# Performance work log

Measured on AMD Instinct MI355X. Metric: run time of the kernel, lower is better.

The kernel has to match this reference:

```python
import jax, jax.numpy as jnp
import numpy as np
import math

EMBED_DIM = 1024
NUM_HEADS = 16
HEAD_DIM = EMBED_DIM // NUM_HEADS
MAX_POSITION = 1024
BATCH = 4
SEQ_LEN = 1024


def setup_inputs() -> dict:
    key = jax.random.key(0)
    ks = jax.random.split(key, 10)
    s = 1.0 / math.sqrt(EMBED_DIM)
    inp = {
        "x": jax.random.normal(ks[0], (BATCH, SEQ_LEN, EMBED_DIM), dtype=jnp.float32),
        "Wq": jax.random.normal(ks[1], (EMBED_DIM, EMBED_DIM), dtype=jnp.float32) * s,
        "bq": jnp.zeros((EMBED_DIM,), dtype=jnp.float32),
        "Wk": jax.random.normal(ks[2], (EMBED_DIM, EMBED_DIM), dtype=jnp.float32) * s,
        "bk": jnp.zeros((EMBED_DIM,), dtype=jnp.float32),
        "Wv": jax.random.normal(ks[3], (EMBED_DIM, EMBED_DIM), dtype=jnp.float32) * s,
        "bv": jnp.zeros((EMBED_DIM,), dtype=jnp.float32),
        "Wo": jax.random.normal(ks[4], (EMBED_DIM, EMBED_DIM), dtype=jnp.float32) * s,
        "bo": jnp.zeros((EMBED_DIM,), dtype=jnp.float32),
        "rel_key": jax.random.normal(ks[5], (MAX_POSITION, HEAD_DIM), dtype=jnp.float32),
    }
    return inp


def reference(x, Wq, bq, Wk, bk, Wv, bv, Wo, bo, rel_key):
    B, S, E = x.shape
    H, D = NUM_HEADS, HEAD_DIM
    # projections, split heads -> (B, H, S, D)
    Q = (x @ Wq + bq).reshape(B, S, H, D).transpose(0, 2, 1, 3)
    K = (x @ Wk + bk).reshape(B, S, H, D).transpose(0, 2, 1, 3)
    V = (x @ Wv + bv).reshape(B, S, H, D).transpose(0, 2, 1, 3)
    # content scores
    attn_content = jnp.einsum('bhqd,bhkd->bhqk', Q, K)
    # relative-position scores via skew trick
    rel = rel_key[MAX_POSITION - S:, :]              # (S, D)
    QEr = jnp.einsum('bhqd,sd->bhqs', Q, rel)        # (B, H, S, S)
    padded = jnp.pad(QEr, ((0, 0), (0, 0), (0, 0), (1, 0)))  # (B, H, S, S+1)
    Srel = padded.reshape(B, H, S + 1, S)[:, :, 1:, :]       # (B, H, S, S)
    scores = (attn_content + Srel) * (1.0 / math.sqrt(D))
    # causal mask
    mask = jnp.tril(jnp.ones((S, S), dtype=bool))
    scores = jnp.where(mask[None, None], scores, -jnp.inf)
    w = jax.nn.softmax(scores, axis=-1)
    out = jnp.einsum('bhqk,bhkd->bhqd', w, V)
    out = out.transpose(0, 2, 1, 3).reshape(B, S, E)
    return out @ Wo + bo
```

## Files before the change

kernel.cpp:

```cpp
#include <hip/hip_runtime.h>

typedef unsigned short u16;
typedef __attribute__((ext_vector_type(8))) __bf16 bf16x8;
typedef __attribute__((ext_vector_type(4))) float f32x4;
typedef __attribute__((ext_vector_type(4))) u16 u16x4;


__device__ __forceinline__ u16 f2bf(float f) {
  unsigned u = __float_as_uint(f);
  u += 0x7fff + ((u >> 16) & 1);
  return (u16)(u >> 16);
}

__device__ __forceinline__ f32x4 mfma16(bf16x8 a, bf16x8 b, f32x4 c) {
  return __builtin_amdgcn_mfma_f32_16x16x32_bf16(a, b, c, 0, 0, 0);
}

__device__ __forceinline__ void gload16(const void* g, void* l) {
  __builtin_amdgcn_global_load_lds(
      (__attribute__((address_space(1))) unsigned int*)(const_cast<void*>(g)),
      (__attribute__((address_space(3))) unsigned int*)l, 16, 0, 0);
}


__global__ void k_f32_to_bf16(const float* __restrict__ in, u16* __restrict__ out, int n4) {
  int i = blockIdx.x * blockDim.x + threadIdx.x;
  if (i < n4) {
    float4 v = reinterpret_cast<const float4*>(in)[i];
    u16x4 o;
    o.x = f2bf(v.x); o.y = f2bf(v.y); o.z = f2bf(v.z); o.w = f2bf(v.w);
    reinterpret_cast<u16x4*>(out)[i] = o;
  }
}

__global__ void k_prep_small(const float* __restrict__ rel, u16* __restrict__ relb,
                             const float* __restrict__ bq, const float* __restrict__ bk,
                             const float* __restrict__ bv, float* __restrict__ bias) {
  const int bx = blockIdx.x, t = threadIdx.x;
  if (bx < 64) {
    int i = bx * 256 + t;
    float4 v = reinterpret_cast<const float4*>(rel)[i];
    u16x4 o;
    o.x = f2bf(v.x); o.y = f2bf(v.y); o.z = f2bf(v.z); o.w = f2bf(v.w);
    reinterpret_cast<u16x4*>(relb)[i] = o;
  } else {
    int i = (bx - 64) * 256 + t;
    if (i < 3072) bias[i] = (i < 1024) ? bq[i] : (i < 2048 ? bk[i - 1024] : bv[i - 2048]);
  }
}

__global__ void k_transpose_w4(const float* __restrict__ W0, const float* __restrict__ W1,
                               const float* __restrict__ W2, const float* __restrict__ W3,
                               u16* __restrict__ outbase) {
  __shared__ float tile[32][33];
  const int z = blockIdx.z;
  const float* in = (z == 0) ? W0 : (z == 1) ? W1 : (z == 2) ? W2 : W3;
  u16* out = outbase + (size_t)z * 1024 * 1024;
  const int r0 = blockIdx.y * 32, c0 = blockIdx.x * 32;
  const int t = threadIdx.x;
  for (int i = t; i < 1024; i += 256) {
    int r = i >> 5, c = i & 31;
    tile[r][c] = in[(size_t)(r0 + r) * 1024 + c0 + c];
  }
  __syncthreads();
  for (int i = t; i < 1024; i += 256) {
    int r = i >> 5, c = i & 31;
    out[(size_t)(c0 + r) * 1024 + r0 + c] = f2bf(tile[c][r]);
  }
}


template<int MODE>
__global__ __launch_bounds__(256) void k_gemm(
    const u16* __restrict__ A, const u16* __restrict__ B,
    const float* __restrict__ bias, void* __restrict__ Cout,
    u16* __restrict__ Vaux, int M, int N, int Kd)
{
  __shared__ u16 Alds[128 * 32];
  __shared__ u16 Blds[128 * 32];
  const int t = threadIdx.x;
  const int lane = t & 63, wid = t >> 6;
  const int wr = wid >> 1, wc = wid & 1;
  const int l15 = lane & 15, lg = lane >> 4;
  const int m0 = blockIdx.y * 128, n0 = blockIdx.x * 128;
  const int trow = t >> 2;
  const int tcol = (t & 3) * 8;

  const f32x4 fzero = {0.f, 0.f, 0.f, 0.f};
  f32x4 acc[4][4];
#pragma unroll
  for (int i = 0; i < 4; i++)
#pragma unroll
    for (int j = 0; j < 4; j++) acc[i][j] = fzero;

  const size_t aoff0 = (size_t)(m0 + trow) * Kd + tcol;
  const size_t aoff1 = (size_t)(m0 + 64 + trow) * Kd + tcol;
  const size_t boff0 = (size_t)(n0 + trow) * Kd + tcol;
  const size_t boff1 = (size_t)(n0 + 64 + trow) * Kd + tcol;
  u16* la0 = Alds + wid * 512;
  u16* la1 = Alds + 2048 + wid * 512;
  u16* lb0 = Blds + wid * 512;
  u16* lb1 = Blds + 2048 + wid * 512;

  for (int k0 = 0; k0 < Kd; k0 += 32) {
    gload16(A + aoff0 + k0, la0);
    gload16(A + aoff1 + k0, la1);
    gload16(B + boff0 + k0, lb0);
    gload16(B + boff1 + k0, lb1);
    __syncthreads();
    bf16x8 av[4], bv[4];
#pragma unroll
    for (int mi = 0; mi < 4; mi++)
      av[mi] = *reinterpret_cast<const bf16x8*>(Alds + (wr * 64 + mi * 16 + l15) * 32 + lg * 8);
#pragma unroll
    for (int ni = 0; ni < 4; ni++)
      bv[ni] = *reinterpret_cast<const bf16x8*>(Blds + (wc * 64 + ni * 16 + l15) * 32 + lg * 8);
#pragma unroll
    for (int mi = 0; mi < 4; mi++)
#pragma unroll
      for (int ni = 0; ni < 4; ni++)
        acc[mi][ni] = mfma16(av[mi], bv[ni], acc[mi][ni]);
    __syncthreads();
  }

#pragma unroll
  for (int mi = 0; mi < 4; mi++) {
#pragma unroll
    for (int ni = 0; ni < 4; ni++) {
      const int col = n0 + wc * 64 + ni * 16 + l15;
      const float bcol = bias[col];
#pragma unroll
      for (int r = 0; r < 4; r++) {
        const int row = m0 + wr * 64 + mi * 16 + lg * 4 + r;
        const float v = acc[mi][ni][r] + bcol;
        if (MODE == 0) {
          ((float*)Cout)[(size_t)row * N + col] = v;
        } else {
          if (col < 2048) {
            ((u16*)Cout)[(size_t)row * N + col] = f2bf(v);
          } else {
            const int bb = row >> 10, ss = row & 1023;
            Vaux[((size_t)bb * 1024 + (col - 2048)) * 1024 + ss] = f2bf(v);
          }
        }
      }
    }
  }
}


__global__ __launch_bounds__(256, 4) void k_attn(
    const u16* __restrict__ qkv,
    const u16* __restrict__ vt,
    const u16* __restrict__ relb,
    u16* __restrict__ Oout)
{
  __shared__ u16 Klds[64 * 64];
  __shared__ u16 Vlds[64 * 64];
  __shared__ float Sbuf[4][16 * 84];

  const int t = threadIdx.x;
  const int lane = t & 63, w = t >> 6;
  const int l15 = lane & 15, lg = lane >> 4;
  const int blk = blockIdx.x;
  const int bh = blk & 63;
  const int g = blk >> 6;
  const int jq = g >> 2, rq = g & 3;
  const int qbt = (jq == 0) ? (15 - rq) : (jq == 1) ? (8 + rq) : (jq == 2) ? (7 - rq) : rq;
  const int b = bh >> 4, h = bh & 15;
  const int qb = qbt * 64;
  const int qw = qb + w * 16;

  float* Wb = Sbuf[w];
  u16* Pb = (u16*)Sbuf[w];

  const f32x4 fzero = {0.f, 0.f, 0.f, 0.f};

  const size_t qrow = (size_t)(b * 1024 + qw + l15) * 3072 + h * 64;
  bf16x8 aQ0 = *reinterpret_cast<const bf16x8*>(qkv + qrow + lg * 8);
  bf16x8 aQ1 = *reinterpret_cast<const bf16x8*>(qkv + qrow + 32 + lg * 8);

  f32x4 oacc[4];
  float l_r[4];
#pragma unroll
  for (int r = 0; r < 4; r++) { oacc[r] = fzero; l_r[r] = 0.f; }

  const int srow = t >> 3;
  const int scb = ((t & 7) * 16) ^ ((srow & 7) << 4);
  const u16* Ks0 = qkv + (size_t)(b * 1024 + srow) * 3072 + 1024 + h * 64 + (scb >> 1);
  const u16* Ks1 = Ks0 + 32 * 3072;
  const u16* Vs0 = vt + (size_t)(bh * 64 + srow) * 1024 + (scb >> 1);
  const u16* Vs1 = Vs0 + 32 * 1024;
  u16* Kd0 = Klds + t * 8;  u16* Kd1 = Klds + (t + 256) * 8;
  u16* Vd0 = Vlds + t * 8;  u16* Vd1 = Vlds + (t + 256) * 8;

  const int nk = qbt + 1;
  const float SC = 0.125f * 1.44269504f;

  for (int kt = 0; kt < nk; kt++) {
    const int k0 = kt * 64;
    gload16(Ks0 + (size_t)k0 * 3072, Kd0);
    gload16(Ks1 + (size_t)k0 * 3072, Kd1);
    gload16(Vs0 + k0, Vd0);
    gload16(Vs1 + k0, Vd1);
    __syncthreads();

    f32x4 sc4[4];
#pragma unroll
    for (int tt = 0; tt < 4; tt++) sc4[tt] = fzero;
#pragma unroll
    for (int tt = 0; tt < 4; tt++) {
      const int row = tt * 16 + l15;
      const int sw = (row & 7) << 4;
      bf16x8 b0 = *reinterpret_cast<const bf16x8*>((const char*)Klds + row * 128 + ((lg * 16) ^ sw));
      bf16x8 b1 = *reinterpret_cast<const bf16x8*>((const char*)Klds + row * 128 + ((64 + lg * 16) ^ sw));
      sc4[tt] = mfma16(aQ0, b0, sc4[tt]);
      sc4[tt] = mfma16(aQ1, b1, sc4[tt]);
    }

    const int rbase = 1008 + k0 - qw;
#pragma unroll
    for (int wj = 0; wj < 5; wj++) {
      int rr = rbase + wj * 16 + l15;
      rr = rr < 0 ? 0 : (rr > 1023 ? 1023 : rr);
      const u16* rp = relb + rr * 64;
      bf16x8 b0 = *reinterpret_cast<const bf16x8*>(rp + lg * 8);
      bf16x8 b1 = *reinterpret_cast<const bf16x8*>(rp + 32 + lg * 8);
      f32x4 z = fzero;
      z = mfma16(aQ0, b0, z);
      z = mfma16(aQ1, b1, z);
#pragma unroll
      for (int r = 0; r < 4; r++)
        Wb[(lg * 4 + r) * 84 + wj * 16 + l15] = z[r];
    }
    __builtin_amdgcn_wave_barrier();

    float pvv[4][4];
#pragma unroll
    for (int r = 0; r < 4; r++) {
      const int rowi = lg * 4 + r;
      const int q = qw + rowi;
      const float* wrow = Wb + rowi * 84 + (15 - rowi);
#pragma unroll
      for (int tt = 0; tt < 4; tt++) {
        const int kg = k0 + tt * 16 + l15;
        float s = (sc4[tt][r] + wrow[tt * 16 + l15]) * SC;
        s = (kg <= q) ? s : -1e30f;
        float p = exp2f(s);
        pvv[tt][r] = p;
        l_r[r] += p;
      }
    }
    __builtin_amdgcn_wave_barrier();
    asm volatile("" ::: "memory");

#pragma unroll
    for (int tt = 0; tt < 4; tt++)
#pragma unroll
      for (int r = 0; r < 4; r++) {
        const int rowi = lg * 4 + r;
        const int cb = (32 * tt + 2 * l15) ^ ((rowi & 7) << 4);
        *(u16*)((char*)Pb + rowi * 128 + cb) = f2bf(pvv[tt][r]);
      }
    __builtin_amdgcn_wave_barrier();

#pragma unroll
    for (int s = 0; s < 2; s++) {
      const int acb = (s * 64 + lg * 16) ^ ((l15 & 7) << 4);
      bf16x8 aP = *reinterpret_cast<const bf16x8*>((const char*)Pb + l15 * 128 + acb);
#pragma unroll
      for (int dt = 0; dt < 4; dt++) {
        const int vrow = dt * 16 + l15;
        const int vcb = (s * 64 + lg * 16) ^ ((vrow & 7) << 4);
        bf16x8 bV = *reinterpret_cast<const bf16x8*>((const char*)Vlds + vrow * 128 + vcb);
        oacc[dt] = mfma16(aP, bV, oacc[dt]);
      }
    }
    __syncthreads();
  }

#pragma unroll
  for (int r = 0; r < 4; r++) {
    float l = l_r[r];
#pragma unroll
    for (int xm = 1; xm < 16; xm <<= 1) l += __shfl_xor(l, xm);
    const float inv = 1.f / l;
    const int q = qw + lg * 4 + r;
#pragma unroll
    for (int dt = 0; dt < 4; dt++)
      Oout[(size_t)(b * 1024 + q) * 1024 + h * 64 + dt * 16 + l15] = f2bf(oacc[dt][r] * inv);
  }
}


extern "C" void kernel_launch(void* const* d_in, const int* in_sizes, int n_in,
                              void* d_out, int out_size, void* d_ws, size_t ws_size,
                              hipStream_t stream) {
  const float* x   = (const float*)d_in[0];
  const float* Wq  = (const float*)d_in[1];
  const float* bq  = (const float*)d_in[2];
  const float* Wk  = (const float*)d_in[3];
  const float* bk  = (const float*)d_in[4];
  const float* Wv  = (const float*)d_in[5];
  const float* bv  = (const float*)d_in[6];
  const float* Wo  = (const float*)d_in[7];
  const float* bo  = (const float*)d_in[8];
  const float* rel = (const float*)d_in[9];

  const size_t MB = 1024 * 1024;
  char* ws = (char*)d_ws;
  u16*   xb    = (u16*)(ws);
  u16*   Wt    = (u16*)(ws + 8 * MB);
  u16*   qkvb  = (u16*)(ws + 16 * MB);
  u16*   vtb   = (u16*)(ws + 40 * MB);
  u16*   relbb = (u16*)(ws + 48 * MB);
  float* bqkv  = (float*)(ws + 49 * MB);
  u16*   Ob    = xb;

  k_f32_to_bf16<<<4096, 256, 0, stream>>>(x, xb, 1048576);
  k_prep_small<<<76, 256, 0, stream>>>(rel, relbb, bq, bk, bv, bqkv);
  k_transpose_w4<<<dim3(32, 32, 4), 256, 0, stream>>>(Wq, Wk, Wv, Wo, Wt);

  k_gemm<2><<<dim3(24, 32), 256, 0, stream>>>(xb, Wt, bqkv, qkvb, vtb, 4096, 3072, 1024);

  k_attn<<<1024, 256, 0, stream>>>(qkvb, vtb, relbb, Ob);

  k_gemm<0><<<dim3(8, 32), 256, 0, stream>>>(Ob, Wt + 3 * MB, bo, d_out, nullptr, 4096, 1024, 1024);
}
```

Measured before the change: 150.2 us.

## Double-buffer K/V/rel tiles in LDS and replace skew buffer with shuffles

The attention kernel now prefetches the next K, V and relative-position key tiles into double-buffered LDS while the current tile is computed, instead of loading and then synchronizing each iteration. The relative-key rows are staged in LDS with a swizzle, replacing per-lane global loads. The skew of the relative scores is done with lane shuffles rather than a round trip through an LDS scratch buffer, and probabilities are written straight to LDS. LDS use roughly doubles, so launch bounds drop to 2 blocks per CU, which trades occupancy for latency hiding.

```diff
diff --git a/kernel.cpp b/kernel.cpp
--- a/kernel.cpp
+++ b/kernel.cpp
@@ -149,15 +149,16 @@
 }
 
 
-__global__ __launch_bounds__(256, 4) void k_attn(
+__global__ __launch_bounds__(256, 2) void k_attn(
     const u16* __restrict__ qkv,
     const u16* __restrict__ vt,
     const u16* __restrict__ relb,
     u16* __restrict__ Oout)
 {
-  __shared__ u16 Klds[64 * 64];
-  __shared__ u16 Vlds[64 * 64];
-  __shared__ float Sbuf[4][16 * 84];
+  __shared__ u16 Klds[2][64 * 64];
+  __shared__ u16 Vlds[2][64 * 64];
+  __shared__ u16 Rlds[2][128 * 64];
+  __shared__ u16 Plds[4][16 * 64];
 
   const int t = threadIdx.x;
   const int lane = t & 63, w = t >> 6;
@@ -171,9 +172,7 @@
   const int qb = qbt * 64;
   const int qw = qb + w * 16;
 
-  float* Wb = Sbuf[w];
-  u16* Pb = (u16*)Sbuf[w];
-
+  u16* Pb = Plds[w];
   const f32x4 fzero = {0.f, 0.f, 0.f, 0.f};
 
   const size_t qrow = (size_t)(b * 1024 + qw + l15) * 3072 + h * 64;
@@ -191,20 +190,54 @@
   const u16* Ks1 = Ks0 + 32 * 3072;
   const u16* Vs0 = vt + (size_t)(bh * 64 + srow) * 1024 + (scb >> 1);
   const u16* Vs1 = Vs0 + 32 * 1024;
-  u16* Kd0 = Klds + t * 8;  u16* Kd1 = Klds + (t + 256) * 8;
-  u16* Vd0 = Vlds + t * 8;  u16* Vd1 = Vlds + (t + 256) * 8;
+
+  const int rstart = 1008 - qb - 48;
+  int rrow[4], rcol[4];
+#pragma unroll
+  for (int ci = 0; ci < 4; ci++) {
+    const int c = t + 256 * ci;
+    rrow[ci] = rstart + (c >> 3);
+    rcol[ci] = ((((c & 7) * 16) ^ (((c >> 3) & 7) << 4)) >> 1);
+  }
 
   const int nk = qbt + 1;
   const float SC = 0.125f * 1.44269504f;
 
+  gload16(Ks0, Klds[0] + t * 8);
+  gload16(Ks1, Klds[0] + (t + 256) * 8);
+  gload16(Vs0, Vlds[0] + t * 8);
+  gload16(Vs1, Vlds[0] + (t + 256) * 8);
+#pragma unroll
+  for (int ci = 0; ci < 4; ci++) {
+    int pr = rrow[ci];
+    pr = pr < 0 ? 0 : (pr > 1023 ? 1023 : pr);
+    gload16(relb + (size_t)pr * 64 + rcol[ci], Rlds[0] + (t + 256 * ci) * 8);
+  }
+  __syncthreads();
+
+  int cur = 0;
   for (int kt = 0; kt < nk; kt++) {
     const int k0 = kt * 64;
-    gload16(Ks0 + (size_t)k0 * 3072, Kd0);
-    gload16(Ks1 + (size_t)k0 * 3072, Kd1);
-    gload16(Vs0 + k0, Vd0);
-    gload16(Vs1 + k0, Vd1);
-    __syncthreads();
-
+
+    if (kt + 1 < nk) {
+      const int kn = k0 + 64;
+      u16* kb = Klds[cur ^ 1];
+      u16* vb = Vlds[cur ^ 1];
+      u16* rb = Rlds[cur ^ 1];
+      gload16(Ks0 + (size_t)kn * 3072, kb + t * 8);
+      gload16(Ks1 + (size_t)kn * 3072, kb + (t + 256) * 8);
+      gload16(Vs0 + kn, vb + t * 8);
+      gload16(Vs1 + kn, vb + (t + 256) * 8);
+#pragma unroll
+      for (int ci = 0; ci < 4; ci++) {
+        int pr = rrow[ci] + kn;
+        pr = pr < 0 ? 0 : (pr > 1023 ? 1023 : pr);
+        gload16(relb + (size_t)pr * 64 + rcol[ci], rb + (t + 256 * ci) * 8);
+      }
+    }
+
+
+    const char* Kb = (const char*)Klds[cur];
     f32x4 sc4[4];
 #pragma unroll
     for (int tt = 0; tt < 4; tt++) sc4[tt] = fzero;
@@ -212,58 +245,50 @@
     for (int tt = 0; tt < 4; tt++) {
       const int row = tt * 16 + l15;
       const int sw = (row & 7) << 4;
-      bf16x8 b0 = *reinterpret_cast<const bf16x8*>((const char*)Klds + row * 128 + ((lg * 16) ^ sw));
-      bf16x8 b1 = *reinterpret_cast<const bf16x8*>((const char*)Klds + row * 128 + ((64 + lg * 16) ^ sw));
+      bf16x8 b0 = *reinterpret_cast<const bf16x8*>(Kb + row * 128 + ((lg * 16) ^ sw));
+      bf16x8 b1 = *reinterpret_cast<const bf16x8*>(Kb + row * 128 + ((64 + lg * 16) ^ sw));
       sc4[tt] = mfma16(aQ0, b0, sc4[tt]);
       sc4[tt] = mfma16(aQ1, b1, sc4[tt]);
     }
 
-    const int rbase = 1008 + k0 - qw;
+    const char* Rb = (const char*)Rlds[cur];
+    f32x4 z[5];
 #pragma unroll
     for (int wj = 0; wj < 5; wj++) {
-      int rr = rbase + wj * 16 + l15;
-      rr = rr < 0 ? 0 : (rr > 1023 ? 1023 : rr);
-      const u16* rp = relb + rr * 64;
-      bf16x8 b0 = *reinterpret_cast<const bf16x8*>(rp + lg * 8);
-      bf16x8 b1 = *reinterpret_cast<const bf16x8*>(rp + 32 + lg * 8);
-      f32x4 z = fzero;
-      z = mfma16(aQ0, b0, z);
-      z = mfma16(aQ1, b1, z);
-#pragma unroll
-      for (int r = 0; r < 4; r++)
-        Wb[(lg * 4 + r) * 84 + wj * 16 + l15] = z[r];
-    }
-    __builtin_amdgcn_wave_barrier();
-
-    float pvv[4][4];
+      const int pr = 48 - 16 * w + wj * 16 + l15;
+      const int sw = (pr & 7) << 4;
+      bf16x8 b0 = *reinterpret_cast<const bf16x8*>(Rb + pr * 128 + ((lg * 16) ^ sw));
+      bf16x8 b1 = *reinterpret_cast<const bf16x8*>(Rb + pr * 128 + ((64 + lg * 16) ^ sw));
+      f32x4 zz = fzero;
+      zz = mfma16(aQ0, b0, zz);
+      zz = mfma16(aQ1, b1, zz);
+      z[wj] = zz;
+    }
+
 #pragma unroll
     for (int r = 0; r < 4; r++) {
       const int rowi = lg * 4 + r;
       const int q = qw + rowi;
-      const float* wrow = Wb + rowi * 84 + (15 - rowi);
+      const int u = l15 + 15 - rowi;
+      const int src = (lane & 48) | (u & 15);
+      float sz[5];
+#pragma unroll
+      for (int wj = 0; wj < 5; wj++) sz[wj] = __shfl(z[wj][r], src);
 #pragma unroll
       for (int tt = 0; tt < 4; tt++) {
         const int kg = k0 + tt * 16 + l15;
-        float s = (sc4[tt][r] + wrow[tt * 16 + l15]) * SC;
-        s = (kg <= q) ? s : -1e30f;
-        float p = exp2f(s);
-        pvv[tt][r] = p;
+        const float wv = (u & 16) ? sz[tt + 1] : sz[tt];
+        const float s = (sc4[tt][r] + wv) * SC;
+        const float p = (kg <= q) ? exp2f(s) : 0.f;
         l_r[r] += p;
+        const int cb = (32 * tt + 2 * l15) ^ ((rowi & 7) << 4);
+        *(u16*)((char*)Pb + rowi * 128 + cb) = f2bf(p);
       }
     }
     __builtin_amdgcn_wave_barrier();
     asm volatile("" ::: "memory");
 
-#pragma unroll
-    for (int tt = 0; tt < 4; tt++)
-#pragma unroll
-      for (int r = 0; r < 4; r++) {
-        const int rowi = lg * 4 + r;
-        const int cb = (32 * tt + 2 * l15) ^ ((rowi & 7) << 4);
-        *(u16*)((char*)Pb + rowi * 128 + cb) = f2bf(pvv[tt][r]);
-      }
-    __builtin_amdgcn_wave_barrier();
-
+    const char* Vb = (const char*)Vlds[cur];
 #pragma unroll
     for (int s = 0; s < 2; s++) {
       const int acb = (s * 64 + lg * 16) ^ ((l15 & 7) << 4);
@@ -272,11 +297,12 @@
       for (int dt = 0; dt < 4; dt++) {
         const int vrow = dt * 16 + l15;
         const int vcb = (s * 64 + lg * 16) ^ ((vrow & 7) << 4);
-        bf16x8 bV = *reinterpret_cast<const bf16x8*>((const char*)Vlds + vrow * 128 + vcb);
+        bf16x8 bV = *reinterpret_cast<const bf16x8*>(Vb + vrow * 128 + vcb);
         oacc[dt] = mfma16(aP, bV, oacc[dt]);
       }
     }
     __syncthreads();
+    cur ^= 1;
   }
 
 #pragma unroll
```

New measurement: 180.1 us. +19.9%, slower.

## Halve attention block to 32 queries and compute rel-pos skew via lane shuffles

Applied to the files above, without the earlier changes.

The attention kernel now uses 128-thread blocks covering 32 query rows each and launches twice as many blocks, processed in descending order of causal work. The relative-position skew, previously done by writing fp32 scores to shared memory and reading them back, is now done with cross-lane shuffles, so the fp32 scratch buffer shrinks to a small bf16 P tile. Exp and the bf16 store to P are fused into one loop. This lowers shared-memory use and improves causal load balance, at the cost of each block reloading K/V tiles for fewer queries, which raises total global traffic.

```diff
diff --git a/kernel.cpp b/kernel.cpp
--- a/kernel.cpp
+++ b/kernel.cpp
@@ -149,7 +149,7 @@
 }
 
 
-__global__ __launch_bounds__(256, 4) void k_attn(
+__global__ __launch_bounds__(128, 4) void k_attn(
     const u16* __restrict__ qkv,
     const u16* __restrict__ vt,
     const u16* __restrict__ relb,
@@ -157,7 +157,7 @@
 {
   __shared__ u16 Klds[64 * 64];
   __shared__ u16 Vlds[64 * 64];
-  __shared__ float Sbuf[4][16 * 84];
+  __shared__ u16 Plds[2][16 * 64];
 
   const int t = threadIdx.x;
   const int lane = t & 63, w = t >> 6;
@@ -165,15 +165,12 @@
   const int blk = blockIdx.x;
   const int bh = blk & 63;
   const int g = blk >> 6;
-  const int jq = g >> 2, rq = g & 3;
-  const int qbt = (jq == 0) ? (15 - rq) : (jq == 1) ? (8 + rq) : (jq == 2) ? (7 - rq) : rq;
+  const int j = 31 - g;
   const int b = bh >> 4, h = bh & 15;
-  const int qb = qbt * 64;
+  const int qb = j * 32;
   const int qw = qb + w * 16;
 
-  float* Wb = Sbuf[w];
-  u16* Pb = (u16*)Sbuf[w];
-
+  u16* Pb = Plds[w];
   const f32x4 fzero = {0.f, 0.f, 0.f, 0.f};
 
   const size_t qrow = (size_t)(b * 1024 + qw + l15) * 3072 + h * 64;
@@ -188,21 +185,18 @@
   const int srow = t >> 3;
   const int scb = ((t & 7) * 16) ^ ((srow & 7) << 4);
   const u16* Ks0 = qkv + (size_t)(b * 1024 + srow) * 3072 + 1024 + h * 64 + (scb >> 1);
-  const u16* Ks1 = Ks0 + 32 * 3072;
   const u16* Vs0 = vt + (size_t)(bh * 64 + srow) * 1024 + (scb >> 1);
-  const u16* Vs1 = Vs0 + 32 * 1024;
-  u16* Kd0 = Klds + t * 8;  u16* Kd1 = Klds + (t + 256) * 8;
-  u16* Vd0 = Vlds + t * 8;  u16* Vd1 = Vlds + (t + 256) * 8;
-
-  const int nk = qbt + 1;
+
+  const int nk = (j >> 1) + 1;
   const float SC = 0.125f * 1.44269504f;
 
   for (int kt = 0; kt < nk; kt++) {
     const int k0 = kt * 64;
-    gload16(Ks0 + (size_t)k0 * 3072, Kd0);
-    gload16(Ks1 + (size_t)k0 * 3072, Kd1);
-    gload16(Vs0 + k0, Vd0);
-    gload16(Vs1 + k0, Vd1);
+#pragma unroll
+    for (int ci = 0; ci < 4; ci++) {
+      gload16(Ks0 + (size_t)(k0 + 16 * ci) * 3072, Klds + (t + 128 * ci) * 8);
+      gload16(Vs0 + (size_t)(16384 * ci) + k0,     Vlds + (t + 128 * ci) * 8);
+    }
     __syncthreads();
 
     f32x4 sc4[4];
@@ -219,6 +213,7 @@
     }
 
     const int rbase = 1008 + k0 - qw;
+    f32x4 z[5];
 #pragma unroll
     for (int wj = 0; wj < 5; wj++) {
       int rr = rbase + wj * 16 + l15;
@@ -226,43 +221,34 @@
       const u16* rp = relb + rr * 64;
       bf16x8 b0 = *reinterpret_cast<const bf16x8*>(rp + lg * 8);
       bf16x8 b1 = *reinterpret_cast<const bf16x8*>(rp + 32 + lg * 8);
-      f32x4 z = fzero;
-      z = mfma16(aQ0, b0, z);
-      z = mfma16(aQ1, b1, z);
-#pragma unroll
-      for (int r = 0; r < 4; r++)
-        Wb[(lg * 4 + r) * 84 + wj * 16 + l15] = z[r];
-    }
-    __builtin_amdgcn_wave_barrier();
-
-    float pvv[4][4];
+      f32x4 zz = fzero;
+      zz = mfma16(aQ0, b0, zz);
+      zz = mfma16(aQ1, b1, zz);
+      z[wj] = zz;
+    }
+
 #pragma unroll
     for (int r = 0; r < 4; r++) {
       const int rowi = lg * 4 + r;
       const int q = qw + rowi;
-      const float* wrow = Wb + rowi * 84 + (15 - rowi);
+      const int u = l15 + 15 - rowi;
+      const int src = (lane & 48) | (u & 15);
+      float sz[5];
+#pragma unroll
+      for (int wj = 0; wj < 5; wj++) sz[wj] = __shfl(z[wj][r], src);
 #pragma unroll
       for (int tt = 0; tt < 4; tt++) {
         const int kg = k0 + tt * 16 + l15;
-        float s = (sc4[tt][r] + wrow[tt * 16 + l15]) * SC;
-        s = (kg <= q) ? s : -1e30f;
-        float p = exp2f(s);
-        pvv[tt][r] = p;
+        const float wv = (u & 16) ? sz[tt + 1] : sz[tt];
+        const float s = (sc4[tt][r] + wv) * SC;
+        const float p = (kg <= q) ? exp2f(s) : 0.f;
         l_r[r] += p;
+        const int cb = (32 * tt + 2 * l15) ^ ((rowi & 7) << 4);
+        *(u16*)((char*)Pb + rowi * 128 + cb) = f2bf(p);
       }
     }
     __builtin_amdgcn_wave_barrier();
     asm volatile("" ::: "memory");
-
-#pragma unroll
-    for (int tt = 0; tt < 4; tt++)
-#pragma unroll
-      for (int r = 0; r < 4; r++) {
-        const int rowi = lg * 4 + r;
-        const int cb = (32 * tt + 2 * l15) ^ ((rowi & 7) << 4);
-        *(u16*)((char*)Pb + rowi * 128 + cb) = f2bf(pvv[tt][r]);
-      }
-    __builtin_amdgcn_wave_barrier();
 
 #pragma unroll
     for (int s = 0; s < 2; s++) {
@@ -323,7 +309,7 @@
 
   k_gemm<2><<<dim3(24, 32), 256, 0, stream>>>(xb, Wt, bqkv, qkvb, vtb, 4096, 3072, 1024);
 
-  k_attn<<<1024, 256, 0, stream>>>(qkvb, vtb, relbb, Ob);
+  k_attn<<<2048, 128, 0, stream>>>(qkvb, vtb, relbb, Ob);
 
   k_gemm<0><<<dim3(8, 32), 256, 0, stream>>>(Ob, Wt + 3 * MB, bo, d_out, nullptr, 4096, 1024, 1024);
 }
```

After: 193.1 us. 28.5% more time.
